# Optimization experiments

Measured on AMD Instinct MI355X. Metric: run time of the kernel, lower is better.

Reference implementation:

```python
import jax, jax.numpy as jnp
import numpy as np

NUM_HEADS = 8


def setup_inputs() -> dict:
    key = jax.random.key(0)
    ks = jax.random.split(key, 8)
    B, S, D = 2, 4096, 512
    # Linear weights init uniform(-0.1, 0.1), no bias; stored as [in, out]
    u = lambda k, shp: jax.random.uniform(k, shp, jnp.float32, -0.1, 0.1)
    return {
        "query_antecedent": jax.random.normal(ks[0], (B, S, D), jnp.float32),
        "memory_antecedent": jax.random.normal(ks[1], (B, S, D), jnp.float32),
        "bias": jax.random.normal(ks[2], (1, S, S), jnp.float32),
        "Wq": u(ks[3], (D, D)),
        "Wk": u(ks[4], (D, D)),
        "Wv": u(ks[5], (D, D)),
        "Wo": u(ks[6], (D, D)),
    }


def reference(query_antecedent, memory_antecedent, bias, Wq, Wk, Wv, Wo):
    B, S, D = query_antecedent.shape
    H = NUM_HEADS
    hd = D // H
    scale = hd ** (-0.5)
    q = (query_antecedent @ Wq) * scale              # [B,S,D]
    k = memory_antecedent @ Wk                       # [B,S,D]
    v = memory_antecedent @ Wv                       # [B,S,D]
    q = q.reshape(B, S, H, hd)
    k = k.reshape(B, S, H, hd)
    v = v.reshape(B, S, H, hd)
    # per-head logits with shared bias (broadcast over batch and heads)
    logits = jnp.einsum("bqhd,bkhd->bhqk", q, k) + bias[:, None, :, :]
    weights = jax.nn.softmax(logits, axis=-1)        # [B,H,S,S]
    out = jnp.einsum("bhqk,bkhd->bqhd", weights, v).reshape(B, S, D)
    return out @ Wo
```

## Files before the change

### kernel.cpp

```cpp
#include <hip/hip_runtime.h>
#include <hip/hip_bf16.h>

typedef __attribute__((ext_vector_type(8))) __bf16 bf16x8;
typedef __attribute__((ext_vector_type(4))) __bf16 bf16x4;
typedef __attribute__((ext_vector_type(4))) float f32x4;
typedef __attribute__((ext_vector_type(2))) unsigned u32x2;
typedef __attribute__((ext_vector_type(4))) unsigned u32x4;

#define LOG2E 1.4426950408889634f
#define FIXED_M 16.0f

static __device__ __forceinline__ f32x4 mfma16(bf16x8 a, bf16x8 b, f32x4 c) {
  return __builtin_amdgcn_mfma_f32_16x16x32_bf16(a, b, c, 0, 0, 0);
}

static __device__ __forceinline__ void gload_lds16(const void* g, void* l) {
  __builtin_amdgcn_global_load_lds(
      (const __attribute__((address_space(1))) unsigned int*)g,
      (__attribute__((address_space(3))) unsigned int*)l, 16, 0, 0);
}

__global__ __launch_bounds__(256) void k_cvt(const float* __restrict__ in,
                                             __bf16* __restrict__ out, int n4) {
  for (int i = blockIdx.x * blockDim.x + threadIdx.x; i < n4;
       i += gridDim.x * blockDim.x) {
    float4 v = reinterpret_cast<const float4*>(in)[i];
    bf16x4 o = {(__bf16)v.x, (__bf16)v.y, (__bf16)v.z, (__bf16)v.w};
    reinterpret_cast<bf16x4*>(out)[i] = o;
  }
}

__global__ __launch_bounds__(256) void k_wt(const float* __restrict__ W,
                                            __bf16* __restrict__ Wt) {
  __shared__ float tile[64][65];
  int bx = blockIdx.x;
  int by = blockIdx.y;
  int tid = threadIdx.x;
#pragma unroll
  for (int p = 0; p < 16; p++) {
    int idx = p * 256 + tid;
    int r = idx >> 6, c = idx & 63;
    tile[r][c] = W[(size_t)(by * 64 + r) * 512 + bx * 64 + c];
  }
  __syncthreads();
#pragma unroll
  for (int p = 0; p < 16; p++) {
    int idx = p * 256 + tid;
    int rn = idx >> 6, ck = idx & 63;
    Wt[(size_t)(bx * 64 + rn) * 512 + by * 64 + ck] = (__bf16)tile[ck][rn];
  }
}

template <int OUT_MODE>
__global__ __launch_bounds__(256) void k_gemm(const __bf16* __restrict__ A,
                                              const __bf16* __restrict__ Bt,
                                              void* __restrict__ Cout,
                                              float scale) {
  constexpr bool SWAP = (OUT_MODE != 2);
  __shared__ __bf16 As[128][72];
  __shared__ __bf16 Bs[64][72];
  const int tid = threadIdx.x;
  const int wid = tid >> 6, lane = tid & 63;
  const int g = lane >> 4, c = lane & 15;
  const int m0 = blockIdx.x * 128, n0 = blockIdx.y * 64;
  const int wr = wid >> 1, wc = wid & 1;

  f32x4 acc[4][2];
#pragma unroll
  for (int i = 0; i < 4; i++)
#pragma unroll
    for (int j = 0; j < 2; j++) acc[i][j] = (f32x4){0.f, 0.f, 0.f, 0.f};

  for (int k0 = 0; k0 < 512; k0 += 64) {
#pragma unroll
    for (int q = 0; q < 4; q++) {
      int idx = (q * 256 + tid) * 8;
      int r = idx >> 6, cc = idx & 63;
      bf16x8 v = *reinterpret_cast<const bf16x8*>(A + (size_t)(m0 + r) * 512 + k0 + cc);
      *reinterpret_cast<bf16x8*>(&As[r][cc]) = v;
    }
#pragma unroll
    for (int q = 0; q < 2; q++) {
      int idx = (q * 256 + tid) * 8;
      int r = idx >> 6, cc = idx & 63;
      bf16x8 v = *reinterpret_cast<const bf16x8*>(Bt + (size_t)(n0 + r) * 512 + k0 + cc);
      *reinterpret_cast<bf16x8*>(&Bs[r][cc]) = v;
    }
    __syncthreads();
#pragma unroll
    for (int kk = 0; kk < 2; kk++) {
      bf16x8 bfrag[2];
#pragma unroll
      for (int nf = 0; nf < 2; nf++)
        bfrag[nf] = *reinterpret_cast<const bf16x8*>(&Bs[wc * 32 + nf * 16 + c][kk * 32 + g * 8]);
#pragma unroll
      for (int mf = 0; mf < 4; mf++) {
        bf16x8 afrag = *reinterpret_cast<const bf16x8*>(&As[wr * 64 + mf * 16 + c][kk * 32 + g * 8]);
#pragma unroll
        for (int nf = 0; nf < 2; nf++)
          acc[mf][nf] = SWAP ? mfma16(bfrag[nf], afrag, acc[mf][nf])
                             : mfma16(afrag, bfrag[nf], acc[mf][nf]);
      }
    }
    __syncthreads();
  }
#pragma unroll
  for (int mf = 0; mf < 4; mf++)
#pragma unroll
    for (int nf = 0; nf < 2; nf++) {
      if (OUT_MODE == 0) {
        int mm = m0 + wr * 64 + mf * 16 + c;
        int nnb = n0 + wc * 32 + nf * 16 + g * 4;
        int b = mm >> 12, s = mm & 4095, h = nnb >> 6, d = nnb & 63;
        bf16x4 ov = {(__bf16)(acc[mf][nf][0] * scale), (__bf16)(acc[mf][nf][1] * scale),
                     (__bf16)(acc[mf][nf][2] * scale), (__bf16)(acc[mf][nf][3] * scale)};
        *reinterpret_cast<bf16x4*>((__bf16*)Cout + ((((size_t)b * 8 + h) * 4096) + s) * 64 + d) = ov;
      } else if (OUT_MODE == 1) {
        int mm = m0 + wr * 64 + mf * 16 + c;
        int nnb = n0 + wc * 32 + nf * 16 + g * 4;
        f32x4 ov = acc[mf][nf] * scale;
        *reinterpret_cast<f32x4*>((float*)Cout + (size_t)mm * 512 + nnb) = ov;
      } else {
        int mmb = m0 + wr * 64 + mf * 16 + g * 4;
        int nn = n0 + wc * 32 + nf * 16 + c;
        int b = mmb >> 12, s = mmb & 4095, h = nn >> 6, d = nn & 63;
        bf16x4 ov = {(__bf16)(acc[mf][nf][0] * scale), (__bf16)(acc[mf][nf][1] * scale),
                     (__bf16)(acc[mf][nf][2] * scale), (__bf16)(acc[mf][nf][3] * scale)};
        *reinterpret_cast<bf16x4*>((__bf16*)Cout + (((size_t)b * 8 + h) * 64 + d) * 4096 + s) = ov;
      }
    }
}

__global__ __launch_bounds__(256, 2) void k_attn(const __bf16* __restrict__ Q,
                                                 const __bf16* __restrict__ K,
                                                 const __bf16* __restrict__ Vt,
                                                 const float* __restrict__ bias,
                                                 __bf16* __restrict__ Out) {
  __shared__ __bf16 KVs[2][2][64][64];

  const int qb = blockIdx.x, bh = blockIdx.y;
  const int b = bh >> 3, h = bh & 7;
  const int tid = threadIdx.x, wid = tid >> 6, lane = tid & 63;
  const int g = lane >> 4, c = lane & 15;
  const int swz = (c & 7) << 4;
  const char* Kb = (const char*)(K + (size_t)bh * 4096 * 64);
  const char* Vb = (const char*)(Vt + (size_t)bh * 64 * 4096);
  const __bf16* Qh = Q + (size_t)bh * 4096 * 64;
  const int q0 = qb * 128 + wid * 32;
  const int myq0 = q0 + c, myq1 = q0 + 16 + c;

  auto stage = [&](int db, int chunk) {
    const int reg = wid >> 1;
    char* dst0 = (char*)&KVs[db][reg][0][0] + (wid & 1) * 4096;
#pragma unroll
    for (int j = 0; j < 4; j++) {
      int Lp = (wid & 1) * 4096 + j * 1024 + lane * 16;
      int L = Lp ^ (((Lp >> 7) & 7) << 4);
      const char* src = (reg == 0)
          ? Kb + (size_t)chunk * 8192 + L
          : Vb + (size_t)(L >> 7) * 8192 + (size_t)chunk * 128 + (L & 127);
      gload_lds16(src, dst0 + j * 1024);
    }
  };

  const float* brow0 = bias + (size_t)myq0 * 4096;
  const float* brow1 = bias + (size_t)myq1 * 4096;

#define LOADB(dst, chunk)                                                      \
  {                                                                            \
    _Pragma("unroll") for (int f = 0; f < 4; f++) dst[0][f] =                  \
        *reinterpret_cast<const f32x4*>(brow0 + (chunk) * 64 + f * 16 + g * 4);\
    _Pragma("unroll") for (int f = 0; f < 4; f++) dst[1][f] =                  \
        *reinterpret_cast<const f32x4*>(brow1 + (chunk) * 64 + f * 16 + g * 4);\
  }

  bf16x8 qa[2][2];
  qa[0][0] = *reinterpret_cast<const bf16x8*>(Qh + (size_t)myq0 * 64 + g * 8);
  qa[0][1] = *reinterpret_cast<const bf16x8*>(Qh + (size_t)myq0 * 64 + 32 + g * 8);
  qa[1][0] = *reinterpret_cast<const bf16x8*>(Qh + (size_t)myq1 * 64 + g * 8);
  qa[1][1] = *reinterpret_cast<const bf16x8*>(Qh + (size_t)myq1 * 64 + 32 + g * 8);

  f32x4 lacc[2];
  lacc[0] = (f32x4){0.f, 0.f, 0.f, 0.f};
  lacc[1] = (f32x4){0.f, 0.f, 0.f, 0.f};
  f32x4 o[2][4];
#pragma unroll
  for (int qt = 0; qt < 2; qt++)
#pragma unroll
    for (int f = 0; f < 4; f++) o[qt][f] = (f32x4){0.f, 0.f, 0.f, 0.f};

  f32x4 bA[2][4], bB[2][4];
  const float NM = -FIXED_M * LOG2E;

  auto process = [&](int db, f32x4 (&bv)[2][4]) {
    asm volatile("s_waitcnt vmcnt(12)" ::: "memory");
    __builtin_amdgcn_s_barrier();
    const char* Kl = (const char*)&KVs[db][0][0][0];
    const char* Vl = (const char*)&KVs[db][1][0][0];
    f32x4 st[2][4];
    __builtin_amdgcn_s_setprio(1);
#pragma unroll
    for (int f = 0; f < 4; f++) {
      const char* rb = Kl + (f * 16 + c) * 128;
      bf16x8 k0 = *reinterpret_cast<const bf16x8*>(rb + ((g * 16) ^ swz));
      bf16x8 k1 = *reinterpret_cast<const bf16x8*>(rb + ((64 + g * 16) ^ swz));
      st[0][f] = mfma16(k1, qa[0][1], mfma16(k0, qa[0][0], bv[0][f]));
      st[1][f] = mfma16(k1, qa[1][1], mfma16(k0, qa[1][0], bv[1][f]));
    }
    __builtin_amdgcn_s_setprio(0);
    bf16x8 vf[2][4];
#pragma unroll
    for (int kk = 0; kk < 2; kk++)
#pragma unroll
      for (int fd = 0; fd < 4; fd++) {
        const char* rb = Vl + (fd * 16 + c) * 128;
        u32x2 lo = *reinterpret_cast<const u32x2*>(rb + ((kk * 64 + g * 8) ^ swz));
        u32x2 hi = *reinterpret_cast<const u32x2*>(rb + ((kk * 64 + 32 + g * 8) ^ swz));
        u32x4 w = {lo[0], lo[1], hi[0], hi[1]};
        vf[kk][fd] = __builtin_bit_cast(bf16x8, w);
      }
#pragma unroll
    for (int qt = 0; qt < 2; qt++) {
#pragma unroll
      for (int f = 0; f < 4; f++) {
#pragma unroll
        for (int r = 0; r < 4; r++)
          st[qt][f][r] = __builtin_exp2f(__builtin_fmaf(st[qt][f][r], LOG2E, NM));
        lacc[qt] += st[qt][f];
      }
      __builtin_amdgcn_s_setprio(1);
#pragma unroll
      for (int kk = 0; kk < 2; kk++) {
        bf16x8 pf = {(__bf16)st[qt][2 * kk][0],     (__bf16)st[qt][2 * kk][1],
                     (__bf16)st[qt][2 * kk][2],     (__bf16)st[qt][2 * kk][3],
                     (__bf16)st[qt][2 * kk + 1][0], (__bf16)st[qt][2 * kk + 1][1],
                     (__bf16)st[qt][2 * kk + 1][2], (__bf16)st[qt][2 * kk + 1][3]};
#pragma unroll
        for (int fd = 0; fd < 4; fd++)
          o[qt][fd] = mfma16(vf[kk][fd], pf, o[qt][fd]);
      }
      __builtin_amdgcn_s_setprio(0);
    }
    __builtin_amdgcn_s_barrier();
  };

  stage(0, 0);
  asm volatile("" ::: "memory");
  stage(1, 1);
  asm volatile("" ::: "memory");
  LOADB(bA, 0);
  asm volatile("" ::: "memory");
  LOADB(bB, 1);
  asm volatile("" ::: "memory");

  for (int t = 0; t < 64; t += 2) {
    process(0, bA);
    stage(0, (t + 2) & 63);
    asm volatile("" ::: "memory");
    LOADB(bA, ((t + 2) & 63));
    asm volatile("" ::: "memory");
    process(1, bB);
    stage(1, (t + 3) & 63);
    asm volatile("" ::: "memory");
    LOADB(bB, ((t + 3) & 63));
    asm volatile("" ::: "memory");
  }

#pragma unroll
  for (int qt = 0; qt < 2; qt++) {
    float l = lacc[qt][0] + lacc[qt][1] + lacc[qt][2] + lacc[qt][3];
    l += __shfl_xor(l, 16);
    l += __shfl_xor(l, 32);
    float inv = 1.f / l;
    int myq = (qt == 0) ? myq0 : myq1;
    __bf16* Orow = Out + ((size_t)b * 4096 + myq) * 512 + h * 64;
#pragma unroll
    for (int fd = 0; fd < 4; fd++) {
      bf16x4 ov = {(__bf16)(o[qt][fd][0] * inv), (__bf16)(o[qt][fd][1] * inv),
                   (__bf16)(o[qt][fd][2] * inv), (__bf16)(o[qt][fd][3] * inv)};
      *reinterpret_cast<bf16x4*>(Orow + fd * 16 + g * 4) = ov;
    }
  }
#undef LOADB
}

extern "C" void kernel_launch(void* const* d_in, const int* in_sizes, int n_in,
                              void* d_out, int out_size, void* d_ws, size_t ws_size,
                              hipStream_t stream) {
  const float* xq = (const float*)d_in[0];
  const float* xm = (const float*)d_in[1];
  const float* bias = (const float*)d_in[2];
  const float* Wq = (const float*)d_in[3];
  const float* Wk = (const float*)d_in[4];
  const float* Wv = (const float*)d_in[5];
  const float* Wo = (const float*)d_in[6];

  const size_t MB = 1024 * 1024;
  char* ws = (char*)d_ws;
  __bf16* xq_b = (__bf16*)(ws + 0);
  __bf16* xm_b = (__bf16*)(ws + 8 * MB);
  __bf16* wqt = (__bf16*)(ws + 16 * MB);
  __bf16* wkt = (__bf16*)(ws + 16 * MB + 524288);
  __bf16* wvt = (__bf16*)(ws + 17 * MB);
  __bf16* wot = (__bf16*)(ws + 17 * MB + 524288);
  __bf16* Qb = (__bf16*)(ws + 18 * MB);
  __bf16* Kb = (__bf16*)(ws + 26 * MB);
  __bf16* AOb = (__bf16*)(ws + 34 * MB);
  __bf16* Vtb = (__bf16*)(ws + 42 * MB);
  if (ws_size < 50 * MB) return;

  const int n4 = 8192 * 512 / 4;
  k_cvt<<<2048, 256, 0, stream>>>(xq, xq_b, n4);
  k_cvt<<<2048, 256, 0, stream>>>(xm, xm_b, n4);
  k_wt<<<dim3(8, 8), 256, 0, stream>>>(Wq, wqt);
  k_wt<<<dim3(8, 8), 256, 0, stream>>>(Wk, wkt);
  k_wt<<<dim3(8, 8), 256, 0, stream>>>(Wv, wvt);
  k_wt<<<dim3(8, 8), 256, 0, stream>>>(Wo, wot);

  k_gemm<0><<<dim3(64, 8), 256, 0, stream>>>(xq_b, wqt, Qb, 0.125f);
  k_gemm<0><<<dim3(64, 8), 256, 0, stream>>>(xm_b, wkt, Kb, 1.0f);
  k_gemm<2><<<dim3(64, 8), 256, 0, stream>>>(xm_b, wvt, Vtb, 1.0f);

  k_attn<<<dim3(32, 16), 256, 0, stream>>>(Qb, Kb, Vtb, bias, AOb);

  k_gemm<1><<<dim3(64, 8), 256, 0, stream>>>(AOb, wot, d_out, 1.0f);
}
```

Before: 229.6 us.

## Share bias tile across both batches per block and remap grid for L2 locality

Each attention block now handles 64 queries for one head across both batch elements instead of 128 queries for one (batch, head). Each bias row is therefore loaded once and reused for both batches, halving bias register traffic per query. The grid is flattened with a remapping so that blocks sharing query rows (different heads) are adjacent, which should improve L2 reuse of the large bias matrix. The cost is doubled LDS (two batches of K/V staged per step) and twice as many K/V loads per block, which may reduce occupancy or add memory pressure.

```diff
diff --git a/kernel.cpp b/kernel.cpp
--- a/kernel.cpp
+++ b/kernel.cpp
@@ -136,108 +136,110 @@
                                                  const __bf16* __restrict__ Vt,
                                                  const float* __restrict__ bias,
                                                  __bf16* __restrict__ Out) {
-  __shared__ __bf16 KVs[2][2][64][64];
-
-  const int qb = blockIdx.x, bh = blockIdx.y;
-  const int b = bh >> 3, h = bh & 7;
+  __shared__ __bf16 KVs[2][2][2][64][64];
+
+  const int id = blockIdx.x;
+  const int qb = ((id >> 6) << 3) | (id & 7);
+  const int h = (id >> 3) & 7;
   const int tid = threadIdx.x, wid = tid >> 6, lane = tid & 63;
   const int g = lane >> 4, c = lane & 15;
   const int swz = (c & 7) << 4;
-  const char* Kb = (const char*)(K + (size_t)bh * 4096 * 64);
-  const char* Vb = (const char*)(Vt + (size_t)bh * 64 * 4096);
-  const __bf16* Qh = Q + (size_t)bh * 4096 * 64;
-  const int q0 = qb * 128 + wid * 32;
-  const int myq0 = q0 + c, myq1 = q0 + 16 + c;
+  const char* KbP[2] = {(const char*)(K + (size_t)h * 4096 * 64),
+                        (const char*)(K + (size_t)(8 + h) * 4096 * 64)};
+  const char* VbP[2] = {(const char*)(Vt + (size_t)h * 64 * 4096),
+                        (const char*)(Vt + (size_t)(8 + h) * 64 * 4096)};
+  const int q0 = qb * 64 + wid * 16;
+  const int myq = q0 + c;
 
   auto stage = [&](int db, int chunk) {
-    const int reg = wid >> 1;
-    char* dst0 = (char*)&KVs[db][reg][0][0] + (wid & 1) * 4096;
-#pragma unroll
-    for (int j = 0; j < 4; j++) {
-      int Lp = (wid & 1) * 4096 + j * 1024 + lane * 16;
+    const int bt = wid >> 1, reg = wid & 1;
+    char* dst0 = (char*)&KVs[db][bt][reg][0][0];
+#pragma unroll
+    for (int j = 0; j < 8; j++) {
+      int Lp = j * 1024 + lane * 16;
       int L = Lp ^ (((Lp >> 7) & 7) << 4);
       const char* src = (reg == 0)
-          ? Kb + (size_t)chunk * 8192 + L
-          : Vb + (size_t)(L >> 7) * 8192 + (size_t)chunk * 128 + (L & 127);
+          ? KbP[bt] + (size_t)chunk * 8192 + L
+          : VbP[bt] + (size_t)(L >> 7) * 8192 + (size_t)chunk * 128 + (L & 127);
       gload_lds16(src, dst0 + j * 1024);
     }
   };
 
-  const float* brow0 = bias + (size_t)myq0 * 4096;
-  const float* brow1 = bias + (size_t)myq1 * 4096;
+  const float* brow = bias + (size_t)myq * 4096;
 
 #define LOADB(dst, chunk)                                                      \
   {                                                                            \
-    _Pragma("unroll") for (int f = 0; f < 4; f++) dst[0][f] =                  \
-        *reinterpret_cast<const f32x4*>(brow0 + (chunk) * 64 + f * 16 + g * 4);\
-    _Pragma("unroll") for (int f = 0; f < 4; f++) dst[1][f] =                  \
-        *reinterpret_cast<const f32x4*>(brow1 + (chunk) * 64 + f * 16 + g * 4);\
+    _Pragma("unroll") for (int f = 0; f < 4; f++) dst[f] =                     \
+        *reinterpret_cast<const f32x4*>(brow + (chunk) * 64 + f * 16 + g * 4); \
   }
 
   bf16x8 qa[2][2];
-  qa[0][0] = *reinterpret_cast<const bf16x8*>(Qh + (size_t)myq0 * 64 + g * 8);
-  qa[0][1] = *reinterpret_cast<const bf16x8*>(Qh + (size_t)myq0 * 64 + 32 + g * 8);
-  qa[1][0] = *reinterpret_cast<const bf16x8*>(Qh + (size_t)myq1 * 64 + g * 8);
-  qa[1][1] = *reinterpret_cast<const bf16x8*>(Qh + (size_t)myq1 * 64 + 32 + g * 8);
+  {
+    const __bf16* Qh0 = Q + (size_t)h * 4096 * 64;
+    const __bf16* Qh1 = Q + (size_t)(8 + h) * 4096 * 64;
+    qa[0][0] = *reinterpret_cast<const bf16x8*>(Qh0 + (size_t)myq * 64 + g * 8);
+    qa[0][1] = *reinterpret_cast<const bf16x8*>(Qh0 + (size_t)myq * 64 + 32 + g * 8);
+    qa[1][0] = *reinterpret_cast<const bf16x8*>(Qh1 + (size_t)myq * 64 + g * 8);
+    qa[1][1] = *reinterpret_cast<const bf16x8*>(Qh1 + (size_t)myq * 64 + 32 + g * 8);
+  }
 
   f32x4 lacc[2];
   lacc[0] = (f32x4){0.f, 0.f, 0.f, 0.f};
   lacc[1] = (f32x4){0.f, 0.f, 0.f, 0.f};
   f32x4 o[2][4];
 #pragma unroll
-  for (int qt = 0; qt < 2; qt++)
-#pragma unroll
-    for (int f = 0; f < 4; f++) o[qt][f] = (f32x4){0.f, 0.f, 0.f, 0.f};
-
-  f32x4 bA[2][4], bB[2][4];
+  for (int bt = 0; bt < 2; bt++)
+#pragma unroll
+    for (int f = 0; f < 4; f++) o[bt][f] = (f32x4){0.f, 0.f, 0.f, 0.f};
+
+  f32x4 bA[4], bB[4];
   const float NM = -FIXED_M * LOG2E;
 
-  auto process = [&](int db, f32x4 (&bv)[2][4]) {
+  auto process = [&](int db, f32x4 (&bv)[4]) {
     asm volatile("s_waitcnt vmcnt(12)" ::: "memory");
     __builtin_amdgcn_s_barrier();
-    const char* Kl = (const char*)&KVs[db][0][0][0];
-    const char* Vl = (const char*)&KVs[db][1][0][0];
-    f32x4 st[2][4];
-    __builtin_amdgcn_s_setprio(1);
-#pragma unroll
-    for (int f = 0; f < 4; f++) {
-      const char* rb = Kl + (f * 16 + c) * 128;
-      bf16x8 k0 = *reinterpret_cast<const bf16x8*>(rb + ((g * 16) ^ swz));
-      bf16x8 k1 = *reinterpret_cast<const bf16x8*>(rb + ((64 + g * 16) ^ swz));
-      st[0][f] = mfma16(k1, qa[0][1], mfma16(k0, qa[0][0], bv[0][f]));
-      st[1][f] = mfma16(k1, qa[1][1], mfma16(k0, qa[1][0], bv[1][f]));
-    }
-    __builtin_amdgcn_s_setprio(0);
-    bf16x8 vf[2][4];
-#pragma unroll
-    for (int kk = 0; kk < 2; kk++)
-#pragma unroll
-      for (int fd = 0; fd < 4; fd++) {
-        const char* rb = Vl + (fd * 16 + c) * 128;
-        u32x2 lo = *reinterpret_cast<const u32x2*>(rb + ((kk * 64 + g * 8) ^ swz));
-        u32x2 hi = *reinterpret_cast<const u32x2*>(rb + ((kk * 64 + 32 + g * 8) ^ swz));
-        u32x4 w = {lo[0], lo[1], hi[0], hi[1]};
-        vf[kk][fd] = __builtin_bit_cast(bf16x8, w);
-      }
-#pragma unroll
-    for (int qt = 0; qt < 2; qt++) {
+#pragma unroll
+    for (int bt = 0; bt < 2; bt++) {
+      const char* Kl = (const char*)&KVs[db][bt][0][0][0];
+      const char* Vl = (const char*)&KVs[db][bt][1][0][0];
+      f32x4 st[4];
+      __builtin_amdgcn_s_setprio(1);
 #pragma unroll
       for (int f = 0; f < 4; f++) {
+        const char* rb = Kl + (f * 16 + c) * 128;
+        bf16x8 k0 = *reinterpret_cast<const bf16x8*>(rb + ((g * 16) ^ swz));
+        bf16x8 k1 = *reinterpret_cast<const bf16x8*>(rb + ((64 + g * 16) ^ swz));
+        st[f] = mfma16(k1, qa[bt][1], mfma16(k0, qa[bt][0], bv[f]));
+      }
+      __builtin_amdgcn_s_setprio(0);
+      bf16x8 vf[2][4];
+#pragma unroll
+      for (int kk = 0; kk < 2; kk++)
+#pragma unroll
+        for (int fd = 0; fd < 4; fd++) {
+          const char* rb = Vl + (fd * 16 + c) * 128;
+          u32x2 lo = *reinterpret_cast<const u32x2*>(rb + ((kk * 64 + g * 8) ^ swz));
+          u32x2 hi = *reinterpret_cast<const u32x2*>(rb + ((kk * 64 + 32 + g * 8) ^ swz));
+          u32x4 w = {lo[0], lo[1], hi[0], hi[1]};
+          vf[kk][fd] = __builtin_bit_cast(bf16x8, w);
+        }
+#pragma unroll
+      for (int f = 0; f < 4; f++) {
 #pragma unroll
         for (int r = 0; r < 4; r++)
-          st[qt][f][r] = __builtin_exp2f(__builtin_fmaf(st[qt][f][r], LOG2E, NM));
-        lacc[qt] += st[qt][f];
+          st[f][r] = __builtin_exp2f(__builtin_fmaf(st[f][r], LOG2E, NM));
+        lacc[bt] += st[f];
       }
       __builtin_amdgcn_s_setprio(1);
 #pragma unroll
       for (int kk = 0; kk < 2; kk++) {
-        bf16x8 pf = {(__bf16)st[qt][2 * kk][0],     (__bf16)st[qt][2 * kk][1],
-                     (__bf16)st[qt][2 * kk][2],     (__bf16)st[qt][2 * kk][3],
-                     (__bf16)st[qt][2 * kk + 1][0], (__bf16)st[qt][2 * kk + 1][1],
-                     (__bf16)st[qt][2 * kk + 1][2], (__bf16)st[qt][2 * kk + 1][3]};
+        bf16x8 pf = {(__bf16)st[2 * kk][0],     (__bf16)st[2 * kk][1],
+                     (__bf16)st[2 * kk][2],     (__bf16)st[2 * kk][3],
+                     (__bf16)st[2 * kk + 1][0], (__bf16)st[2 * kk + 1][1],
+                     (__bf16)st[2 * kk + 1][2], (__bf16)st[2 * kk + 1][3]};
 #pragma unroll
         for (int fd = 0; fd < 4; fd++)
-          o[qt][fd] = mfma16(vf[kk][fd], pf, o[qt][fd]);
+          o[bt][fd] = mfma16(vf[kk][fd], pf, o[bt][fd]);
       }
       __builtin_amdgcn_s_setprio(0);
     }
@@ -267,17 +269,16 @@
   }
 
 #pragma unroll
-  for (int qt = 0; qt < 2; qt++) {
-    float l = lacc[qt][0] + lacc[qt][1] + lacc[qt][2] + lacc[qt][3];
+  for (int bt = 0; bt < 2; bt++) {
+    float l = lacc[bt][0] + lacc[bt][1] + lacc[bt][2] + lacc[bt][3];
     l += __shfl_xor(l, 16);
     l += __shfl_xor(l, 32);
     float inv = 1.f / l;
-    int myq = (qt == 0) ? myq0 : myq1;
-    __bf16* Orow = Out + ((size_t)b * 4096 + myq) * 512 + h * 64;
+    __bf16* Orow = Out + ((size_t)bt * 4096 + myq) * 512 + h * 64;
 #pragma unroll
     for (int fd = 0; fd < 4; fd++) {
-      bf16x4 ov = {(__bf16)(o[qt][fd][0] * inv), (__bf16)(o[qt][fd][1] * inv),
-                   (__bf16)(o[qt][fd][2] * inv), (__bf16)(o[qt][fd][3] * inv)};
+      bf16x4 ov = {(__bf16)(o[bt][fd][0] * inv), (__bf16)(o[bt][fd][1] * inv),
+                   (__bf16)(o[bt][fd][2] * inv), (__bf16)(o[bt][fd][3] * inv)};
       *reinterpret_cast<bf16x4*>(Orow + fd * 16 + g * 4) = ov;
     }
   }
@@ -321,7 +322,7 @@
   k_gemm<0><<<dim3(64, 8), 256, 0, stream>>>(xm_b, wkt, Kb, 1.0f);
   k_gemm<2><<<dim3(64, 8), 256, 0, stream>>>(xm_b, wvt, Vtb, 1.0f);
 
-  k_attn<<<dim3(32, 16), 256, 0, stream>>>(Qb, Kb, Vtb, bias, AOb);
+  k_attn<<<512, 256, 0, stream>>>(Qb, Kb, Vtb, bias, AOb);
 
   k_gemm<1><<<dim3(64, 8), 256, 0, stream>>>(AOb, wot, d_out, 1.0f);
 }
```

Result: no change. 229.3 us (-0.1%).
